# Kernel optimization log

Hardware: AMD Instinct MI355X
Metric: run time of the kernel (lower is better)

The kernel has to match this reference:

```python
import jax, jax.numpy as jnp
import numpy as np

B, N, D = 64, 1024, 768


def setup_inputs() -> dict:
    key = jax.random.key(0)
    kq, kk, kv = jax.random.split(key, 3)
    Q = jax.random.normal(kq, (B, N, D), dtype=jnp.float32)
    K = jax.random.normal(kk, (B, N, D), dtype=jnp.float32)
    V = jax.random.normal(kv, (B, N, D), dtype=jnp.float32)
    # nn.Parameter(torch.ones(1) * dim ** 0.5)
    temperature = jnp.ones((1,), dtype=jnp.float32) * (D ** 0.5)
    return {"Q": Q, "K": K, "V": V, "temperature": temperature}


def reference(Q, K, V, temperature):
    # scores: [B, N, N]
    scores = jnp.einsum("bqd,bkd->bqk", Q, K) / temperature[0]
    n = scores.shape[-1]
    diag = jnp.eye(n, dtype=bool)  # diagonal self-exclusion mask
    scores = jnp.where(diag[None, :, :], -jnp.inf, scores)
    attn = jax.nn.softmax(scores, axis=-1)
    out = jnp.einsum("bqk,bkd->bqd", attn, V)
    return out
```

## Files before the change

### kernel.cpp

```cpp
#include <hip/hip_runtime.h>


typedef __bf16 bf16x8 __attribute__((ext_vector_type(8)));
typedef __bf16 bf16x4 __attribute__((ext_vector_type(4)));
typedef float  f32x16 __attribute__((ext_vector_type(16)));
typedef float  f32x4v __attribute__((ext_vector_type(4)));

#define WS_Q 0UL
#define WS_K 100663296UL
#define WS_V 201326592UL
#define WS_NEEDED 301989888UL

#define QOFF   0
#define POFF   98304
#define REDOFF 131072
#define LDS_MAIN 135168

__device__ __forceinline__ void gld16(const void* g, const char* l) {
    __builtin_amdgcn_global_load_lds(
        (const __attribute__((address_space(1))) unsigned int*)g,
        (__attribute__((address_space(3))) unsigned int*)(l), 16, 0, 0);
}

__global__ __launch_bounds__(256) void prep_q(const float* __restrict__ Qg,
                                              const float* __restrict__ Tg,
                                              unsigned short* __restrict__ Qws) {
    __shared__ __align__(16) unsigned short L[64 * 72];
    const int bid = blockIdx.x;
    const int tid = threadIdx.x;
    const float scale2 = 1.4426950408889634f / Tg[0];
    const float* src = Qg + (size_t)bid * 64 * 768;
    char* outb = (char*)Qws + (size_t)bid * 98304;
    const int q  = tid >> 2;
    const int k0 = (tid & 3) * 16;
    #pragma unroll 1
    for (int st = 0; st < 12; ++st) {
        #pragma unroll
        for (int i = 0; i < 4; ++i) {
            f32x4v v = *(const f32x4v*)(src + (size_t)q * 768 + st * 64 + k0 + i * 4);
            bf16x4 hb = { (__bf16)(v[0] * scale2), (__bf16)(v[1] * scale2),
                          (__bf16)(v[2] * scale2), (__bf16)(v[3] * scale2) };
            *(bf16x4*)((char*)L + q * 144 + (k0 + i * 4) * 2) = hb;
        }
        __syncthreads();
        #pragma unroll
        for (int i = 0; i < 2; ++i) {
            int u = tid * 2 + i;
            int ks = u >> 7, mrr = (u >> 6) & 1, l = u & 63;
            bf16x8 f = *(const bf16x8*)((char*)L + (mrr * 32 + (l & 31)) * 144
                                        + ks * 32 + 16 * (l >> 5));
            *(bf16x8*)(outb + (size_t)st * 8192 + u * 16) = f;
        }
        __syncthreads();
    }
}

__global__ __launch_bounds__(512) void prep_k(const float* __restrict__ Kg,
                                              unsigned short* __restrict__ Kws) {
    __shared__ __align__(16) unsigned short L[128 * 72];
    const int bid = blockIdx.x;
    const int tid = threadIdx.x;
    const float* src = Kg + (size_t)bid * 128 * 768;
    char* outb = (char*)Kws + (size_t)bid * 196608;
    const int kv = tid >> 2;
    const int k0 = (tid & 3) * 16;
    #pragma unroll 1
    for (int st = 0; st < 12; ++st) {
        #pragma unroll
        for (int i = 0; i < 4; ++i) {
            f32x4v v = *(const f32x4v*)(src + (size_t)kv * 768 + st * 64 + k0 + i * 4);
            bf16x4 hb = { (__bf16)v[0], (__bf16)v[1], (__bf16)v[2], (__bf16)v[3] };
            *(bf16x4*)((char*)L + kv * 144 + (k0 + i * 4) * 2) = hb;
        }
        __syncthreads();
        #pragma unroll
        for (int i = 0; i < 2; ++i) {
            int u = tid * 2 + i;
            int ks = u >> 8, ncc = (u >> 6) & 3, l = u & 63;
            bf16x8 f = *(const bf16x8*)((char*)L + (ncc * 32 + (l & 31)) * 144
                                        + ks * 32 + 16 * (l >> 5));
            *(bf16x8*)(outb + (size_t)st * 16384 + u * 16) = f;
        }
        __syncthreads();
    }
}

__global__ __launch_bounds__(512) void prep_v(const float* __restrict__ Vg,
                                              unsigned short* __restrict__ Vws) {
    __shared__ __align__(16) unsigned short L[128 * 136];
    const int bid = blockIdx.x;
    const int tid = threadIdx.x;
    const float* src = Vg + (size_t)bid * 128 * 768;
    char* outb = (char*)Vws + (size_t)bid * 196608;
    const int srg = tid & 31, scg = tid >> 5;
    #pragma unroll 1
    for (int jg = 0; jg < 6; ++jg) {
        #pragma unroll
        for (int i2 = 0; i2 < 2; ++i2) {
            int cg = scg + i2 * 16;
            const float* vp = src + (size_t)(srg * 4) * 768 + jg * 128 + cg * 4;
            f32x4v a0 = *(const f32x4v*)(vp);
            f32x4v a1 = *(const f32x4v*)(vp + 768);
            f32x4v a2 = *(const f32x4v*)(vp + 1536);
            f32x4v a3 = *(const f32x4v*)(vp + 2304);
            #pragma unroll
            for (int c = 0; c < 4; ++c) {
                int d = cg * 4 + c;
                bf16x4 hb = { (__bf16)a0[c], (__bf16)a1[c], (__bf16)a2[c], (__bf16)a3[c] };
                *(bf16x4*)((char*)L + d * 272 + srg * 8) = hb;
            }
        }
        __syncthreads();
        #pragma unroll
        for (int i = 0; i < 4; ++i) {
            int u = tid * 4 + i;
            int kh = u >> 10, ks = (u >> 8) & 3, ncc = (u >> 6) & 3, l = u & 63;
            bf16x8 f = *(const bf16x8*)((char*)L + (ncc * 32 + (l & 31)) * 272
                                        + kh * 128 + ks * 32 + 16 * (l >> 5));
            *(bf16x8*)(outb + (size_t)(jg * 2 + kh) * 16384 + (u & 1023) * 16) = f;
        }
        __syncthreads();
    }
}

#define OFFK(sl) ((size_t)((sl) >> 2) * 16384 + (size_t)((sl) & 3) * 4096)
#define OFFV(ksl) ((size_t)((ksl) >> 3) * 196608 + (size_t)(((ksl) >> 2) & 1) * 16384 \
                   + (size_t)((ksl) & 3) * 4096)

#define LGKM0_BAR() do {                                            \
    asm volatile("s_waitcnt lgkmcnt(0)" ::: "memory");              \
    __builtin_amdgcn_s_barrier();                                   \
    asm volatile("" ::: "memory"); } while (0)

__global__ __launch_bounds__(512, 2) void lsa_main(
    const unsigned short* __restrict__ Qws, const unsigned short* __restrict__ Kws,
    const unsigned short* __restrict__ Vws, float* __restrict__ Og)
{
    extern __shared__ char sm[];
    const int tid  = threadIdx.x;
    const int lane = tid & 63;
    const int w    = tid >> 6;
    const int hh   = lane >> 5;
    const int l31  = lane & 31;

    int id = blockIdx.x;
    int xcd = id & 7, jj = id >> 3;
    int batch = (jj >> 5) * 16 + xcd * 2 + ((jj >> 4) & 1);
    int qt = jj & 15;

    const char* qimg = (const char*)Qws + (size_t)(batch * 16 + qt) * 98304;
    const char* kimg = (const char*)Kws + (size_t)batch * 1572864;
    const char* vimg = (const char*)Vws + (size_t)batch * 1572864;
    float* redm = (float*)(sm + REDOFF);
    float* redl = (float*)(sm + REDOFF + 2048);

    #pragma unroll
    for (int i = 0; i < 12; ++i)
        gld16(qimg + i * 8192 + tid * 16, sm + QOFF + i * 8192 + w * 1024);
    __syncthreads();

    f32x16 acc[3][2];
    #pragma unroll
    for (int g3 = 0; g3 < 3; ++g3)
        #pragma unroll
        for (int qg = 0; qg < 2; ++qg)
            #pragma unroll
            for (int r = 0; r < 16; ++r) acc[g3][qg][r] = 0.0f;
    float m_st[2] = { -3e38f, -3e38f };
    float l_st[2] = { 0.0f, 0.0f };

    const size_t kwoff = (size_t)(w >> 2) * 196608 + (size_t)(w & 3) * 1024
                         + (size_t)lane * 16;
    size_t voff3[3];
    #pragma unroll
    for (int g3 = 0; g3 < 3; ++g3) {
        int dgi = w * 3 + g3;
        voff3[g3] = (size_t)(dgi >> 2) * 32768 + (size_t)(dgi & 3) * 1024
                    + (size_t)lane * 16;
    }
    const int diag_t2 = qt >> 2;

    #pragma unroll 1
    for (int t2 = 0; t2 < 4; ++t2) {
        const char* kb = kimg + (size_t)t2 * 393216 + kwoff;
        f32x16 s[2];
        #pragma unroll
        for (int qg = 0; qg < 2; ++qg)
            #pragma unroll
            for (int r = 0; r < 16; ++r) s[qg][r] = 0.0f;

        bf16x8 kr[8];
        #pragma unroll
        for (int j = 0; j < 8; ++j) kr[j] = *(const bf16x8*)(kb + OFFK(j));

        #pragma unroll
        for (int sl = 0; sl < 48; ++sl) {
            bf16x8 kf  = kr[sl & 7];
            bf16x8 qf0 = *(const bf16x8*)(sm + QOFF + (sl * 2 + 0) * 1024 + lane * 16);
            bf16x8 qf1 = *(const bf16x8*)(sm + QOFF + (sl * 2 + 1) * 1024 + lane * 16);
            __builtin_amdgcn_s_setprio(1);
            s[0] = __builtin_amdgcn_mfma_f32_32x32x16_bf16(kf, qf0, s[0], 0, 0, 0);
            s[1] = __builtin_amdgcn_mfma_f32_32x32x16_bf16(kf, qf1, s[1], 0, 0, 0);
            __builtin_amdgcn_s_setprio(0);
            if (sl < 40)
                kr[sl & 7] = *(const bf16x8*)(kb + OFFK(sl + 8));
        }

        const char* vb = vimg + (size_t)t2 * 393216;
        bf16x8 vr[4][3];
        #pragma unroll
        for (int kk = 0; kk < 4; ++kk)
            #pragma unroll
            for (int g3 = 0; g3 < 3; ++g3)
                vr[kk][g3] = *(const bf16x8*)(vb + voff3[g3] + OFFV(kk));

        if (t2 == diag_t2) {
            #pragma unroll
            for (int qg = 0; qg < 2; ++qg)
                #pragma unroll
                for (int r = 0; r < 16; ++r) {
                    int kvg = t2 * 256 + w * 32 + (r & 3) + 8 * (r >> 2) + 4 * hh;
                    if (kvg == qt * 64 + qg * 32 + l31) s[qg][r] = -3e38f;
                }
        }

        #pragma unroll
        for (int qg = 0; qg < 2; ++qg) {
            float pm = s[qg][0];
            #pragma unroll
            for (int r = 1; r < 16; ++r) pm = fmaxf(pm, s[qg][r]);
            pm = fmaxf(pm, __shfl_xor(pm, 32, 64));
            if (hh == 0) redm[(qg * 32 + l31) * 8 + w] = pm;
        }
        LGKM0_BAR();
        float cf[2];
        #pragma unroll
        for (int qg = 0; qg < 2; ++qg) {
            const float* rp = redm + (qg * 32 + l31) * 8;
            f32x4v a = *(const f32x4v*)rp;
            f32x4v b = *(const f32x4v*)(rp + 4);
            float mn = fmaxf(fmaxf(fmaxf(a[0], a[1]), fmaxf(a[2], a[3])),
                             fmaxf(fmaxf(b[0], b[1]), fmaxf(b[2], b[3])));
            mn = fmaxf(mn, m_st[qg]);
            cf[qg] = __builtin_amdgcn_exp2f(m_st[qg] - mn);
            m_st[qg] = mn;
            float pl = 0.0f;
            #pragma unroll
            for (int r = 0; r < 16; ++r) {
                float e = __builtin_amdgcn_exp2f(s[qg][r] - mn);
                s[qg][r] = e; pl += e;
            }
            pl += __shfl_xor(pl, 32, 64);
            l_st[qg] = l_st[qg] * cf[qg] + pl;
        }
        #pragma unroll
        for (int g3 = 0; g3 < 3; ++g3)
            #pragma unroll
            for (int qg = 0; qg < 2; ++qg)
                #pragma unroll
                for (int r = 0; r < 16; ++r) acc[g3][qg][r] *= cf[qg];

        #pragma unroll
        for (int qg = 0; qg < 2; ++qg)
            #pragma unroll
            for (int g = 0; g < 4; ++g) {
                bf16x4 p4 = { (__bf16)s[qg][4 * g + 0], (__bf16)s[qg][4 * g + 1],
                              (__bf16)s[qg][4 * g + 2], (__bf16)s[qg][4 * g + 3] };
                int blk = (2 * w + (g >> 1)) * 2 + qg;
                int lidx = (g & 1) * 32 + l31;
                *(bf16x4*)(sm + POFF + blk * 1024 + lidx * 16 + hh * 8) = p4;
            }
        LGKM0_BAR();

        #pragma unroll
        for (int ksl = 0; ksl < 16; ++ksl) {
            bf16x8 pa0 = *(const bf16x8*)(sm + POFF + (ksl * 2 + 0) * 1024 + lane * 16);
            bf16x8 pa1 = *(const bf16x8*)(sm + POFF + (ksl * 2 + 1) * 1024 + lane * 16);
            __builtin_amdgcn_s_setprio(1);
            #pragma unroll
            for (int g3 = 0; g3 < 3; ++g3) {
                acc[g3][0] = __builtin_amdgcn_mfma_f32_32x32x16_bf16(vr[ksl & 3][g3], pa0, acc[g3][0], 0, 0, 0);
                acc[g3][1] = __builtin_amdgcn_mfma_f32_32x32x16_bf16(vr[ksl & 3][g3], pa1, acc[g3][1], 0, 0, 0);
            }
            __builtin_amdgcn_s_setprio(0);
            if (ksl < 12) {
                #pragma unroll
                for (int g3 = 0; g3 < 3; ++g3)
                    vr[ksl & 3][g3] = *(const bf16x8*)(vb + voff3[g3] + OFFV(ksl + 4));
            }
        }
    }

    #pragma unroll
    for (int qg = 0; qg < 2; ++qg)
        if (hh == 0) redl[(qg * 32 + l31) * 8 + w] = l_st[qg];
    __syncthreads();
    float rinv[2];
    #pragma unroll
    for (int qg = 0; qg < 2; ++qg) {
        const float* rp = redl + (qg * 32 + l31) * 8;
        f32x4v a = *(const f32x4v*)rp;
        f32x4v b = *(const f32x4v*)(rp + 4);
        rinv[qg] = 1.0f / (a[0] + a[1] + a[2] + a[3] + b[0] + b[1] + b[2] + b[3]);
    }

    char* obt = sm + QOFF;
    const size_t orow = (size_t)batch * 1024 + (size_t)qt * 64;
    const int q2 = tid >> 3, c8 = tid & 7;

    #pragma unroll
    for (int g3 = 0; g3 < 3; ++g3) {
        __syncthreads();
        #pragma unroll
        for (int qg = 0; qg < 2; ++qg) {
            int q = qg * 32 + l31;
            int qx = (q & 15) << 4;
            #pragma unroll
            for (int g = 0; g < 4; ++g) {
                f32x4v o4 = { acc[g3][qg][4 * g + 0] * rinv[qg],
                              acc[g3][qg][4 * g + 1] * rinv[qg],
                              acc[g3][qg][4 * g + 2] * rinv[qg],
                              acc[g3][qg][4 * g + 3] * rinv[qg] };
                int dloc = w * 32 + 8 * g + 4 * hh;
                *(f32x4v*)(obt + q * 1024 + ((dloc * 4) ^ qx)) = o4;
            }
        }
        __syncthreads();
        #pragma unroll
        for (int i = 0; i < 8; ++i) {
            int db = c8 * 128 + i * 16;
            f32x4v o = *(const f32x4v*)(obt + q2 * 1024 + (db ^ ((q2 & 15) << 4)));
            int dg = c8 * 96 + g3 * 32 + i * 4;
            *(f32x4v*)(Og + (orow + q2) * 768 + dg) = o;
        }
    }
}

__device__ __forceinline__ void fb_stage_load(f32x4v (&vr)[2][4], const float* __restrict__ Vg,
                                              size_t kvbase, int srg, int scg, int ch) {
    #pragma unroll
    for (int i2 = 0; i2 < 2; ++i2) {
        const float* vp = Vg + kvbase + (size_t)(srg * 4) * 768 + ch * 128 + (scg + i2 * 16) * 4;
        #pragma unroll
        for (int rr = 0; rr < 4; ++rr)
            vr[i2][rr] = *(const f32x4v*)(vp + (size_t)rr * 768);
    }
}
__device__ __forceinline__ void fb_stage_write(const f32x4v (&vr)[2][4], char* Vb, int srg, int scg) {
    #pragma unroll
    for (int i2 = 0; i2 < 2; ++i2) {
        int cg = scg + i2 * 16;
        #pragma unroll
        for (int q4 = 0; q4 < 4; ++q4) {
            int drow = cg * 4 + q4;
            bf16x4 hv = { (__bf16)vr[i2][0][q4], (__bf16)vr[i2][1][q4],
                          (__bf16)vr[i2][2][q4], (__bf16)vr[i2][3][q4] };
            *(bf16x4*)(Vb + drow * 256 + ((srg * 8) ^ ((drow & 15) << 4))) = hv;
        }
    }
}
#define FB_OFF_V  98304
#define FB_OFF_P  131072
#define FB_OFF_RM 147456
#define FB_OFF_RL 148480
#define FB_LDS    149504
__global__ __launch_bounds__(512) void lsa_fb(
    const float* __restrict__ Qg, const float* __restrict__ Kg,
    const float* __restrict__ Vg, const float* __restrict__ Tg,
    float* __restrict__ Og)
{
    extern __shared__ char smem[];
    char*  Qb    = smem;
    char*  Vb    = smem + FB_OFF_V;
    char*  Pb    = smem + FB_OFF_P;
    float* red_m = (float*)(smem + FB_OFF_RM);
    float* red_l = (float*)(smem + FB_OFF_RL);
    const int tid  = threadIdx.x;
    const int lane = tid & 63;
    const int w    = tid >> 6;
    const int mr   = w & 1;
    const int nc   = w >> 1;
    const int half = lane >> 5;
    const int l31  = lane & 31;
    int id = blockIdx.x, xcd = id & 7, jj = id >> 3;
    int batch = (jj >> 5) * 16 + xcd * 2 + ((jj >> 4) & 1);
    int qt = jj & 15;
    const float scale2 = 1.4426950408889634f / Tg[0];
    {
        const float* qp   = Qg + ((size_t)batch * 1024 + (size_t)qt * 64) * 768;
        int   row   = tid >> 3, c0 = tid & 7;
        const float* qrow = qp + (size_t)row * 768;
        char* qdst  = Qb + row * 1536;
        int   rx    = (row & 15) << 4;
        #pragma unroll
        for (int j = 0; j < 24; ++j) {
            int c4 = c0 + j * 8;
            f32x4v q4 = *(const f32x4v*)(qrow + c4 * 4);
            bf16x4 hq = { (__bf16)(q4[0] * scale2), (__bf16)(q4[1] * scale2),
                          (__bf16)(q4[2] * scale2), (__bf16)(q4[3] * scale2) };
            *(bf16x4*)(qdst + ((c4 * 8) ^ rx)) = hq;
        }
    }
    __syncthreads();
    f32x16 acc[6];
    #pragma unroll
    for (int ch = 0; ch < 6; ++ch)
        #pragma unroll
        for (int r = 0; r < 16; ++r) acc[ch][r] = 0.0f;
    float m_st = -3e38f, l_st = 0.0f;
    const int  qrow_g = mr * 32 + l31;
    const int  qglob  = qt * 64 + qrow_g;
    char*      qfbase = Qb + qrow_g * 1536;
    const int  qx     = (qrow_g & 15) << 4;
    char*      pfbase = Pb + qrow_g * 256;
    const int  vrow   = nc * 32 + l31;
    char*      vfbase = Vb + vrow * 256;
    const int  vx     = (vrow & 15) << 4;
    const int  diag_tile = qt >> 1;
    const int  srg = tid & 31, scg = tid >> 5;
    #pragma unroll 1
    for (int t = 0; t < 8; ++t) {
        const size_t kvbase = ((size_t)batch * 1024 + (size_t)t * 128) * 768;
        f32x16 s;
        #pragma unroll
        for (int r = 0; r < 16; ++r) s[r] = 0.0f;
        const float* kptr = Kg + kvbase + (size_t)(nc * 32 + l31) * 768 + 8 * half;
        #pragma unroll
        for (int ch = 0; ch < 6; ++ch) {
            #pragma unroll
            for (int ks = 0; ks < 8; ++ks) {
                f32x4v k0 = *(const f32x4v*)(kptr + ch * 128 + ks * 16);
                f32x4v k1 = *(const f32x4v*)(kptr + ch * 128 + ks * 16 + 4);
                bf16x8 kf = { (__bf16)k0[0], (__bf16)k0[1], (__bf16)k0[2], (__bf16)k0[3],
                              (__bf16)k1[0], (__bf16)k1[1], (__bf16)k1[2], (__bf16)k1[3] };
                bf16x8 qf = *(const bf16x8*)(qfbase + ((ch * 256 + ks * 32 + half * 16) ^ qx));
                s = __builtin_amdgcn_mfma_f32_32x32x16_bf16(kf, qf, s, 0, 0, 0);
            }
        }
        if (t == diag_tile) {
            #pragma unroll
            for (int r = 0; r < 16; ++r) {
                int kvg = t * 128 + nc * 32 + (r & 3) + 8 * (r >> 2) + 4 * half;
                if (kvg == qglob) s[r] = -3e38f;
            }
        }
        f32x4v vr[2][4];
        fb_stage_load(vr, Vg, kvbase, srg, scg, 0);
        float pm = s[0];
        #pragma unroll
        for (int r = 1; r < 16; ++r) pm = fmaxf(pm, s[r]);
        pm = fmaxf(pm, __shfl_xor(pm, 32, 64));
        if (half == 0) red_m[qrow_g * 4 + nc] = pm;
        __syncthreads();
        f32x4v m4 = *(const f32x4v*)(red_m + qrow_g * 4);
        float mnew = fmaxf(fmaxf(m4[0], m4[1]), fmaxf(m4[2], m4[3]));
        mnew = fmaxf(mnew, m_st);
        float cf = __builtin_amdgcn_exp2f(m_st - mnew);
        m_st = mnew;
        float pl = 0.0f;
        #pragma unroll
        for (int r = 0; r < 16; ++r) {
            float e = __builtin_amdgcn_exp2f(s[r] - mnew);
            s[r] = e; pl += e;
        }
        pl += __shfl_xor(pl, 32, 64);
        l_st = l_st * cf + pl;
        #pragma unroll
        for (int ch = 0; ch < 6; ++ch)
            #pragma unroll
            for (int r = 0; r < 16; ++r) acc[ch][r] *= cf;
        #pragma unroll
        for (int g = 0; g < 4; ++g) {
            bf16x4 hp = { (__bf16)s[4*g+0], (__bf16)s[4*g+1],
                          (__bf16)s[4*g+2], (__bf16)s[4*g+3] };
            *(bf16x4*)(pfbase + ((nc * 64 + g * 16 + half * 8) ^ qx)) = hp;
        }
        fb_stage_write(vr, Vb, srg, scg);
        __syncthreads();
        bf16x8 pa[8];
        #pragma unroll
        for (int ks = 0; ks < 8; ++ks)
            pa[ks] = *(const bf16x8*)(pfbase + ((ks * 32 + half * 16) ^ qx));
        #pragma unroll
        for (int ch = 0; ch < 6; ++ch) {
            if (ch < 5) fb_stage_load(vr, Vg, kvbase, srg, scg, ch + 1);
            #pragma unroll
            for (int ks = 0; ks < 8; ++ks) {
                bf16x8 vf = *(const bf16x8*)(vfbase + ((ks * 32 + half * 16) ^ vx));
                acc[ch] = __builtin_amdgcn_mfma_f32_32x32x16_bf16(vf, pa[ks], acc[ch], 0, 0, 0);
            }
            if (ch < 5) {
                __syncthreads();
                fb_stage_write(vr, Vb, srg, scg);
                __syncthreads();
            }
        }
    }
    if (half == 0) red_l[qrow_g * 4 + nc] = l_st;
    __syncthreads();
    f32x4v l4 = *(const f32x4v*)(red_l + qrow_g * 4);
    float rinv = 1.0f / (l4[0] + l4[1] + l4[2] + l4[3]);
    float* op = Og + ((size_t)batch * 1024 + (size_t)qglob) * 768;
    #pragma unroll
    for (int ch = 0; ch < 6; ++ch)
        #pragma unroll
        for (int g = 0; g < 4; ++g) {
            f32x4v o4 = { acc[ch][4*g+0] * rinv, acc[ch][4*g+1] * rinv,
                          acc[ch][4*g+2] * rinv, acc[ch][4*g+3] * rinv };
            *(f32x4v*)(op + ch * 128 + nc * 32 + g * 8 + half * 4) = o4;
        }
}

extern "C" void kernel_launch(void* const* d_in, const int* in_sizes, int n_in,
                              void* d_out, int out_size, void* d_ws, size_t ws_size,
                              hipStream_t stream) {
    (void)in_sizes; (void)n_in; (void)out_size;
    const float* Q = (const float*)d_in[0];
    const float* K = (const float*)d_in[1];
    const float* V = (const float*)d_in[2];
    const float* T = (const float*)d_in[3];
    float* O = (float*)d_out;
    if (ws_size >= WS_NEEDED) {
        unsigned short* Qws = (unsigned short*)((char*)d_ws + WS_Q);
        unsigned short* Kws = (unsigned short*)((char*)d_ws + WS_K);
        unsigned short* Vws = (unsigned short*)((char*)d_ws + WS_V);
        prep_q<<<dim3(1024), dim3(256), 0, stream>>>(Q, T, Qws);
        prep_k<<<dim3(512),  dim3(512), 0, stream>>>(K, Kws);
        prep_v<<<dim3(512),  dim3(512), 0, stream>>>(V, Vws);
        lsa_main<<<dim3(1024), dim3(512), LDS_MAIN, stream>>>(Qws, Kws, Vws, O);
    } else {
        lsa_fb<<<dim3(1024), dim3(512), FB_LDS, stream>>>(Q, K, V, T, O);
    }
}
```

Measured before the change: 493.8 us.

## Merge prep kernels into one launch and widen per-wave KV tile in main loop

Merges the three Q/K/V conversion kernels into a single launch that dispatches on block index, removing two kernel launches and their tail effects. In the attention kernel, each wave now computes a 64-key score slice (two 32-row K fragments) per iteration, so each KV pass covers 512 keys in 2 iterations instead of 256 keys in 4. This halves the max/sum reduction and rescale rounds. The P tile is written to LDS in two halves by lower and upper waves, with extra barriers between. It raises register pressure (more score accumulators) and adds synchronization within each iteration.

```diff
diff --git a/kernel.cpp b/kernel.cpp
--- a/kernel.cpp
+++ b/kernel.cpp
@@ -22,115 +22,110 @@
         (__attribute__((address_space(3))) unsigned int*)(l), 16, 0, 0);
 }
 
-__global__ __launch_bounds__(256) void prep_q(const float* __restrict__ Qg,
-                                              const float* __restrict__ Tg,
-                                              unsigned short* __restrict__ Qws) {
-    __shared__ __align__(16) unsigned short L[64 * 72];
-    const int bid = blockIdx.x;
-    const int tid = threadIdx.x;
-    const float scale2 = 1.4426950408889634f / Tg[0];
-    const float* src = Qg + (size_t)bid * 64 * 768;
-    char* outb = (char*)Qws + (size_t)bid * 98304;
-    const int q  = tid >> 2;
-    const int k0 = (tid & 3) * 16;
-    #pragma unroll 1
-    for (int st = 0; st < 12; ++st) {
-        #pragma unroll
-        for (int i = 0; i < 4; ++i) {
-            f32x4v v = *(const f32x4v*)(src + (size_t)q * 768 + st * 64 + k0 + i * 4);
-            bf16x4 hb = { (__bf16)(v[0] * scale2), (__bf16)(v[1] * scale2),
-                          (__bf16)(v[2] * scale2), (__bf16)(v[3] * scale2) };
-            *(bf16x4*)((char*)L + q * 144 + (k0 + i * 4) * 2) = hb;
-        }
-        __syncthreads();
-        #pragma unroll
-        for (int i = 0; i < 2; ++i) {
-            int u = tid * 2 + i;
-            int ks = u >> 7, mrr = (u >> 6) & 1, l = u & 63;
-            bf16x8 f = *(const bf16x8*)((char*)L + (mrr * 32 + (l & 31)) * 144
-                                        + ks * 32 + 16 * (l >> 5));
-            *(bf16x8*)(outb + (size_t)st * 8192 + u * 16) = f;
-        }
-        __syncthreads();
-    }
-}
-
-__global__ __launch_bounds__(512) void prep_k(const float* __restrict__ Kg,
-                                              unsigned short* __restrict__ Kws) {
-    __shared__ __align__(16) unsigned short L[128 * 72];
-    const int bid = blockIdx.x;
-    const int tid = threadIdx.x;
-    const float* src = Kg + (size_t)bid * 128 * 768;
-    char* outb = (char*)Kws + (size_t)bid * 196608;
-    const int kv = tid >> 2;
-    const int k0 = (tid & 3) * 16;
-    #pragma unroll 1
-    for (int st = 0; st < 12; ++st) {
-        #pragma unroll
-        for (int i = 0; i < 4; ++i) {
-            f32x4v v = *(const f32x4v*)(src + (size_t)kv * 768 + st * 64 + k0 + i * 4);
-            bf16x4 hb = { (__bf16)v[0], (__bf16)v[1], (__bf16)v[2], (__bf16)v[3] };
-            *(bf16x4*)((char*)L + kv * 144 + (k0 + i * 4) * 2) = hb;
-        }
-        __syncthreads();
-        #pragma unroll
-        for (int i = 0; i < 2; ++i) {
-            int u = tid * 2 + i;
-            int ks = u >> 8, ncc = (u >> 6) & 3, l = u & 63;
-            bf16x8 f = *(const bf16x8*)((char*)L + (ncc * 32 + (l & 31)) * 144
-                                        + ks * 32 + 16 * (l >> 5));
-            *(bf16x8*)(outb + (size_t)st * 16384 + u * 16) = f;
-        }
-        __syncthreads();
-    }
-}
-
-__global__ __launch_bounds__(512) void prep_v(const float* __restrict__ Vg,
-                                              unsigned short* __restrict__ Vws) {
-    __shared__ __align__(16) unsigned short L[128 * 136];
-    const int bid = blockIdx.x;
-    const int tid = threadIdx.x;
-    const float* src = Vg + (size_t)bid * 128 * 768;
-    char* outb = (char*)Vws + (size_t)bid * 196608;
-    const int srg = tid & 31, scg = tid >> 5;
-    #pragma unroll 1
-    for (int jg = 0; jg < 6; ++jg) {
-        #pragma unroll
-        for (int i2 = 0; i2 < 2; ++i2) {
-            int cg = scg + i2 * 16;
-            const float* vp = src + (size_t)(srg * 4) * 768 + jg * 128 + cg * 4;
-            f32x4v a0 = *(const f32x4v*)(vp);
-            f32x4v a1 = *(const f32x4v*)(vp + 768);
-            f32x4v a2 = *(const f32x4v*)(vp + 1536);
-            f32x4v a3 = *(const f32x4v*)(vp + 2304);
-            #pragma unroll
-            for (int c = 0; c < 4; ++c) {
-                int d = cg * 4 + c;
-                bf16x4 hb = { (__bf16)a0[c], (__bf16)a1[c], (__bf16)a2[c], (__bf16)a3[c] };
-                *(bf16x4*)((char*)L + d * 272 + srg * 8) = hb;
-            }
-        }
-        __syncthreads();
-        #pragma unroll
-        for (int i = 0; i < 4; ++i) {
-            int u = tid * 4 + i;
-            int kh = u >> 10, ks = (u >> 8) & 3, ncc = (u >> 6) & 3, l = u & 63;
-            bf16x8 f = *(const bf16x8*)((char*)L + (ncc * 32 + (l & 31)) * 272
-                                        + kh * 128 + ks * 32 + 16 * (l >> 5));
-            *(bf16x8*)(outb + (size_t)(jg * 2 + kh) * 16384 + (u & 1023) * 16) = f;
-        }
-        __syncthreads();
-    }
-}
-
-#define OFFK(sl) ((size_t)((sl) >> 2) * 16384 + (size_t)((sl) & 3) * 4096)
-#define OFFV(ksl) ((size_t)((ksl) >> 3) * 196608 + (size_t)(((ksl) >> 2) & 1) * 16384 \
-                   + (size_t)((ksl) & 3) * 4096)
-
 #define LGKM0_BAR() do {                                            \
     asm volatile("s_waitcnt lgkmcnt(0)" ::: "memory");              \
     __builtin_amdgcn_s_barrier();                                   \
     asm volatile("" ::: "memory"); } while (0)
+
+__global__ __launch_bounds__(512) void prep_all(
+    const float* __restrict__ Qg, const float* __restrict__ Kg,
+    const float* __restrict__ Vg, const float* __restrict__ Tg,
+    unsigned short* __restrict__ Qws, unsigned short* __restrict__ Kws,
+    unsigned short* __restrict__ Vws)
+{
+    __shared__ __align__(16) char Lraw[34816];
+    const int bid = blockIdx.x;
+    const int tid = threadIdx.x;
+
+    if (bid < 1024) {
+        const float scale2 = 1.4426950408889634f / Tg[0];
+        const float* src = Qg + (size_t)bid * 49152;
+        char* outb = (char*)Qws + (size_t)bid * 98304;
+        const int row = tid >> 3;
+        const int c0  = tid & 7;
+        #pragma unroll 1
+        for (int st = 0; st < 12; ++st) {
+            #pragma unroll
+            for (int i = 0; i < 2; ++i) {
+                f32x4v v = *(const f32x4v*)(src + (size_t)row * 768 + st * 64 + c0 * 8 + i * 4);
+                bf16x4 hb = { (__bf16)(v[0] * scale2), (__bf16)(v[1] * scale2),
+                              (__bf16)(v[2] * scale2), (__bf16)(v[3] * scale2) };
+                *(bf16x4*)(Lraw + row * 144 + (c0 * 8 + i * 4) * 2) = hb;
+            }
+            __syncthreads();
+            {
+                int u = tid;
+                int ks = u >> 7, mrr = (u >> 6) & 1, l = u & 63;
+                bf16x8 f = *(const bf16x8*)(Lraw + (mrr * 32 + (l & 31)) * 144
+                                            + ks * 32 + 16 * (l >> 5));
+                *(bf16x8*)(outb + (size_t)st * 8192 + u * 16) = f;
+            }
+            __syncthreads();
+        }
+    } else if (bid < 1536) {
+        const int b2 = bid - 1024;
+        const float* src = Kg + (size_t)b2 * 98304;
+        char* outb = (char*)Kws + (size_t)b2 * 196608;
+        const int kv = tid >> 2;
+        const int k0 = (tid & 3) * 16;
+        #pragma unroll 1
+        for (int st = 0; st < 12; ++st) {
+            #pragma unroll
+            for (int i = 0; i < 4; ++i) {
+                f32x4v v = *(const f32x4v*)(src + (size_t)kv * 768 + st * 64 + k0 + i * 4);
+                bf16x4 hb = { (__bf16)v[0], (__bf16)v[1], (__bf16)v[2], (__bf16)v[3] };
+                *(bf16x4*)(Lraw + kv * 144 + (k0 + i * 4) * 2) = hb;
+            }
+            __syncthreads();
+            #pragma unroll
+            for (int i = 0; i < 2; ++i) {
+                int u = tid * 2 + i;
+                int ks = u >> 8, ncc = (u >> 6) & 3, l = u & 63;
+                bf16x8 f = *(const bf16x8*)(Lraw + (ncc * 32 + (l & 31)) * 144
+                                            + ks * 32 + 16 * (l >> 5));
+                *(bf16x8*)(outb + (size_t)st * 16384 + u * 16) = f;
+            }
+            __syncthreads();
+        }
+    } else {
+        const int b2 = bid - 1536;
+        const float* src = Vg + (size_t)b2 * 98304;
+        char* outb = (char*)Vws + (size_t)b2 * 196608;
+        const int srg = tid & 31, scg = tid >> 5;
+        #pragma unroll 1
+        for (int jg = 0; jg < 6; ++jg) {
+            #pragma unroll
+            for (int i2 = 0; i2 < 2; ++i2) {
+                int cg = scg + i2 * 16;
+                const float* vp = src + (size_t)(srg * 4) * 768 + jg * 128 + cg * 4;
+                f32x4v a0 = *(const f32x4v*)(vp);
+                f32x4v a1 = *(const f32x4v*)(vp + 768);
+                f32x4v a2 = *(const f32x4v*)(vp + 1536);
+                f32x4v a3 = *(const f32x4v*)(vp + 2304);
+                #pragma unroll
+                for (int c = 0; c < 4; ++c) {
+                    int d = cg * 4 + c;
+                    bf16x4 hb = { (__bf16)a0[c], (__bf16)a1[c], (__bf16)a2[c], (__bf16)a3[c] };
+                    *(bf16x4*)(Lraw + d * 272 + srg * 8) = hb;
+                }
+            }
+            __syncthreads();
+            #pragma unroll
+            for (int i = 0; i < 4; ++i) {
+                int u = tid * 4 + i;
+                int kh = u >> 10, ks = (u >> 8) & 3, ncc = (u >> 6) & 3, l = u & 63;
+                bf16x8 f = *(const bf16x8*)(Lraw + (ncc * 32 + (l & 31)) * 272
+                                            + kh * 128 + ks * 32 + 16 * (l >> 5));
+                *(bf16x8*)(outb + (size_t)(jg * 2 + kh) * 16384 + (u & 1023) * 16) = f;
+            }
+            __syncthreads();
+        }
+    }
+}
+
+#define OFFK(st)  ((size_t)((st) >> 2) * 16384 + (size_t)((st) & 3) * 4096)
+#define OFFV(ks)  ((size_t)((ks) >> 3) * 196608 + (size_t)(((ks) >> 2) & 1) * 16384 \
+                   + (size_t)((ks) & 3) * 4096)
 
 __global__ __launch_bounds__(512, 2) void lsa_main(
     const unsigned short* __restrict__ Qws, const unsigned short* __restrict__ Kws,
@@ -169,8 +164,8 @@
     float m_st[2] = { -3e38f, -3e38f };
     float l_st[2] = { 0.0f, 0.0f };
 
-    const size_t kwoff = (size_t)(w >> 2) * 196608 + (size_t)(w & 3) * 1024
-                         + (size_t)lane * 16;
+    const char* kbase = kimg + (size_t)(w >> 1) * 196608 + (size_t)(w & 1) * 2048
+                        + (size_t)lane * 16;
     size_t voff3[3];
     #pragma unroll
     for (int g3 = 0; g3 < 3; ++g3) {
@@ -178,57 +173,70 @@
         voff3[g3] = (size_t)(dgi >> 2) * 32768 + (size_t)(dgi & 3) * 1024
                     + (size_t)lane * 16;
     }
-    const int diag_t2 = qt >> 2;
+    const int diag_t2 = qt >> 3;
+    const int wlo = (w < 4);
 
     #pragma unroll 1
-    for (int t2 = 0; t2 < 4; ++t2) {
-        const char* kb = kimg + (size_t)t2 * 393216 + kwoff;
-        f32x16 s[2];
-        #pragma unroll
-        for (int qg = 0; qg < 2; ++qg)
-            #pragma unroll
-            for (int r = 0; r < 16; ++r) s[qg][r] = 0.0f;
-
-        bf16x8 kr[8];
-        #pragma unroll
-        for (int j = 0; j < 8; ++j) kr[j] = *(const bf16x8*)(kb + OFFK(j));
-
-        #pragma unroll
-        for (int sl = 0; sl < 48; ++sl) {
-            bf16x8 kf  = kr[sl & 7];
-            bf16x8 qf0 = *(const bf16x8*)(sm + QOFF + (sl * 2 + 0) * 1024 + lane * 16);
-            bf16x8 qf1 = *(const bf16x8*)(sm + QOFF + (sl * 2 + 1) * 1024 + lane * 16);
-            __builtin_amdgcn_s_setprio(1);
-            s[0] = __builtin_amdgcn_mfma_f32_32x32x16_bf16(kf, qf0, s[0], 0, 0, 0);
-            s[1] = __builtin_amdgcn_mfma_f32_32x32x16_bf16(kf, qf1, s[1], 0, 0, 0);
-            __builtin_amdgcn_s_setprio(0);
-            if (sl < 40)
-                kr[sl & 7] = *(const bf16x8*)(kb + OFFK(sl + 8));
-        }
-
-        const char* vb = vimg + (size_t)t2 * 393216;
-        bf16x8 vr[4][3];
-        #pragma unroll
-        for (int kk = 0; kk < 4; ++kk)
-            #pragma unroll
-            for (int g3 = 0; g3 < 3; ++g3)
-                vr[kk][g3] = *(const bf16x8*)(vb + voff3[g3] + OFFV(kk));
-
-        if (t2 == diag_t2) {
+    for (int t2 = 0; t2 < 2; ++t2) {
+        const char* kb = kbase + (size_t)t2 * 786432;
+        f32x16 s[2][2];
+        #pragma unroll
+        for (int kk = 0; kk < 2; ++kk)
             #pragma unroll
             for (int qg = 0; qg < 2; ++qg)
                 #pragma unroll
-                for (int r = 0; r < 16; ++r) {
-                    int kvg = t2 * 256 + w * 32 + (r & 3) + 8 * (r >> 2) + 4 * hh;
-                    if (kvg == qt * 64 + qg * 32 + l31) s[qg][r] = -3e38f;
-                }
+                for (int r = 0; r < 16; ++r) s[kk][qg][r] = 0.0f;
+
+        bf16x8 kr[2][4];
+        #pragma unroll
+        for (int p = 0; p < 4; ++p) {
+            kr[0][p] = *(const bf16x8*)(kb + OFFK(p));
+            kr[1][p] = *(const bf16x8*)(kb + OFFK(p) + 1024);
+        }
+
+        #pragma unroll
+        for (int st = 0; st < 48; ++st) {
+            bf16x8 qf0 = *(const bf16x8*)(sm + QOFF + (st * 2 + 0) * 1024 + lane * 16);
+            bf16x8 qf1 = *(const bf16x8*)(sm + QOFF + (st * 2 + 1) * 1024 + lane * 16);
+            __builtin_amdgcn_s_setprio(1);
+            s[0][0] = __builtin_amdgcn_mfma_f32_32x32x16_bf16(kr[0][st & 3], qf0, s[0][0], 0, 0, 0);
+            s[0][1] = __builtin_amdgcn_mfma_f32_32x32x16_bf16(kr[0][st & 3], qf1, s[0][1], 0, 0, 0);
+            s[1][0] = __builtin_amdgcn_mfma_f32_32x32x16_bf16(kr[1][st & 3], qf0, s[1][0], 0, 0, 0);
+            s[1][1] = __builtin_amdgcn_mfma_f32_32x32x16_bf16(kr[1][st & 3], qf1, s[1][1], 0, 0, 0);
+            __builtin_amdgcn_s_setprio(0);
+            if (st < 44) {
+                kr[0][st & 3] = *(const bf16x8*)(kb + OFFK(st + 4));
+                kr[1][st & 3] = *(const bf16x8*)(kb + OFFK(st + 4) + 1024);
+            }
+        }
+
+        const char* vbt = vimg + (size_t)t2 * 786432;
+        bf16x8 vrg[2][3];
+        #pragma unroll
+        for (int p = 0; p < 2; ++p)
+            #pragma unroll
+            for (int g3 = 0; g3 < 3; ++g3)
+                vrg[p][g3] = *(const bf16x8*)(vbt + voff3[g3] + OFFV(p));
+
+        if (t2 == diag_t2) {
+            #pragma unroll
+            for (int kk = 0; kk < 2; ++kk)
+                #pragma unroll
+                for (int qg = 0; qg < 2; ++qg)
+                    #pragma unroll
+                    for (int r = 0; r < 16; ++r) {
+                        int kvg = t2 * 512 + w * 64 + kk * 32 + (r & 3) + 8 * (r >> 2) + 4 * hh;
+                        if (kvg == qt * 64 + qg * 32 + l31) s[kk][qg][r] = -3e38f;
+                    }
         }
 
         #pragma unroll
         for (int qg = 0; qg < 2; ++qg) {
-            float pm = s[qg][0];
-            #pragma unroll
-            for (int r = 1; r < 16; ++r) pm = fmaxf(pm, s[qg][r]);
+            float pm = s[0][qg][0];
+            #pragma unroll
+            for (int r = 1; r < 16; ++r) pm = fmaxf(pm, s[0][qg][r]);
+            #pragma unroll
+            for (int r = 0; r < 16; ++r) pm = fmaxf(pm, s[1][qg][r]);
             pm = fmaxf(pm, __shfl_xor(pm, 32, 64));
             if (hh == 0) redm[(qg * 32 + l31) * 8 + w] = pm;
         }
@@ -246,10 +254,12 @@
             m_st[qg] = mn;
             float pl = 0.0f;
             #pragma unroll
-            for (int r = 0; r < 16; ++r) {
-                float e = __builtin_amdgcn_exp2f(s[qg][r] - mn);
-                s[qg][r] = e; pl += e;
-            }
+            for (int kk = 0; kk < 2; ++kk)
+                #pragma unroll
+                for (int r = 0; r < 16; ++r) {
+                    float e = __builtin_amdgcn_exp2f(s[kk][qg][r] - mn);
+                    s[kk][qg][r] = e; pl += e;
+                }
             pl += __shfl_xor(pl, 32, 64);
             l_st[qg] = l_st[qg] * cf[qg] + pl;
         }
@@ -260,35 +270,60 @@
                 #pragma unroll
                 for (int r = 0; r < 16; ++r) acc[g3][qg][r] *= cf[qg];
 
-        #pragma unroll
-        for (int qg = 0; qg < 2; ++qg)
-            #pragma unroll
-            for (int g = 0; g < 4; ++g) {
-                bf16x4 p4 = { (__bf16)s[qg][4 * g + 0], (__bf16)s[qg][4 * g + 1],
-                              (__bf16)s[qg][4 * g + 2], (__bf16)s[qg][4 * g + 3] };
-                int blk = (2 * w + (g >> 1)) * 2 + qg;
-                int lidx = (g & 1) * 32 + l31;
-                *(bf16x4*)(sm + POFF + blk * 1024 + lidx * 16 + hh * 8) = p4;
-            }
+        #define WRITE_P() do {                                                      \
+            _Pragma("unroll")                                                       \
+            for (int kk = 0; kk < 2; ++kk)                                          \
+                _Pragma("unroll")                                                   \
+                for (int g = 0; g < 4; ++g)                                         \
+                    _Pragma("unroll")                                               \
+                    for (int qg = 0; qg < 2; ++qg) {                                \
+                        bf16x4 p4 = { (__bf16)s[kk][qg][4*g+0], (__bf16)s[kk][qg][4*g+1], \
+                                      (__bf16)s[kk][qg][4*g+2], (__bf16)s[kk][qg][4*g+3] }; \
+                        int bidx = (((w & 3) * 4 + kk * 2 + (g >> 1)) * 2 + qg);    \
+                        *(bf16x4*)(sm + POFF + bidx * 1024                          \
+                                   + ((g & 1) * 32 + l31) * 16 + hh * 8) = p4;      \
+                    } } while (0)
+
+        if (wlo) WRITE_P();
         LGKM0_BAR();
 
         #pragma unroll
-        for (int ksl = 0; ksl < 16; ++ksl) {
-            bf16x8 pa0 = *(const bf16x8*)(sm + POFF + (ksl * 2 + 0) * 1024 + lane * 16);
-            bf16x8 pa1 = *(const bf16x8*)(sm + POFF + (ksl * 2 + 1) * 1024 + lane * 16);
+        for (int lk = 0; lk < 16; ++lk) {
+            bf16x8 pa0 = *(const bf16x8*)(sm + POFF + (lk * 2 + 0) * 1024 + lane * 16);
+            bf16x8 pa1 = *(const bf16x8*)(sm + POFF + (lk * 2 + 1) * 1024 + lane * 16);
             __builtin_amdgcn_s_setprio(1);
             #pragma unroll
             for (int g3 = 0; g3 < 3; ++g3) {
-                acc[g3][0] = __builtin_amdgcn_mfma_f32_32x32x16_bf16(vr[ksl & 3][g3], pa0, acc[g3][0], 0, 0, 0);
-                acc[g3][1] = __builtin_amdgcn_mfma_f32_32x32x16_bf16(vr[ksl & 3][g3], pa1, acc[g3][1], 0, 0, 0);
+                acc[g3][0] = __builtin_amdgcn_mfma_f32_32x32x16_bf16(vrg[lk & 1][g3], pa0, acc[g3][0], 0, 0, 0);
+                acc[g3][1] = __builtin_amdgcn_mfma_f32_32x32x16_bf16(vrg[lk & 1][g3], pa1, acc[g3][1], 0, 0, 0);
             }
             __builtin_amdgcn_s_setprio(0);
-            if (ksl < 12) {
+            #pragma unroll
+            for (int g3 = 0; g3 < 3; ++g3)
+                vrg[lk & 1][g3] = *(const bf16x8*)(vbt + voff3[g3] + OFFV(lk + 2));
+        }
+        LGKM0_BAR();
+        if (!wlo) WRITE_P();
+        LGKM0_BAR();
+
+        #pragma unroll
+        for (int lk = 16; lk < 32; ++lk) {
+            bf16x8 pa0 = *(const bf16x8*)(sm + POFF + ((lk - 16) * 2 + 0) * 1024 + lane * 16);
+            bf16x8 pa1 = *(const bf16x8*)(sm + POFF + ((lk - 16) * 2 + 1) * 1024 + lane * 16);
+            __builtin_amdgcn_s_setprio(1);
+            #pragma unroll
+            for (int g3 = 0; g3 < 3; ++g3) {
+                acc[g3][0] = __builtin_amdgcn_mfma_f32_32x32x16_bf16(vrg[lk & 1][g3], pa0, acc[g3][0], 0, 0, 0);
+                acc[g3][1] = __builtin_amdgcn_mfma_f32_32x32x16_bf16(vrg[lk & 1][g3], pa1, acc[g3][1], 0, 0, 0);
+            }
+            __builtin_amdgcn_s_setprio(0);
+            if (lk < 30) {
                 #pragma unroll
                 for (int g3 = 0; g3 < 3; ++g3)
-                    vr[ksl & 3][g3] = *(const bf16x8*)(vb + voff3[g3] + OFFV(ksl + 4));
-            }
-        }
+                    vrg[lk & 1][g3] = *(const bf16x8*)(vbt + voff3[g3] + OFFV(lk + 2));
+            }
+        }
+        #undef WRITE_P
     }
 
     #pragma unroll
@@ -524,9 +559,7 @@
         unsigned short* Qws = (unsigned short*)((char*)d_ws + WS_Q);
         unsigned short* Kws = (unsigned short*)((char*)d_ws + WS_K);
         unsigned short* Vws = (unsigned short*)((char*)d_ws + WS_V);
-        prep_q<<<dim3(1024), dim3(256), 0, stream>>>(Q, T, Qws);
-        prep_k<<<dim3(512),  dim3(512), 0, stream>>>(K, Kws);
-        prep_v<<<dim3(512),  dim3(512), 0, stream>>>(V, Vws);
+        prep_all<<<dim3(2048), dim3(512), 0, stream>>>(Q, K, V, T, Qws, Kws, Vws);
         lsa_main<<<dim3(1024), dim3(512), LDS_MAIN, stream>>>(Qws, Kws, Vws, O);
     } else {
         lsa_fb<<<dim3(1024), dim3(512), FB_LDS, stream>>>(Q, K, V, T, O);
```

Result: no change. 494.1 us (+0.1%).
